# Optimization experiments

Measured on AMD Instinct MI355X. Metric: run time of the kernel, lower is better.

Reference implementation:

```python
import jax, jax.numpy as jnp
import numpy as np

HIDDEN = 768
HEADS = 12
HEAD_DIM = 64
SEQ = 512
DS_K = 64  # downsampling_k
EPS = 1e-6


def setup_inputs() -> dict:
    key = jax.random.key(0)
    ks = jax.random.split(key, 16)
    B = 32
    sd = 1.0 / DS_K
    glorot = jax.nn.initializers.lecun_normal()  # flax default_kernel_init
    inp = {
        "query": jax.random.normal(ks[0], (B, SEQ, HIDDEN), jnp.float32),
        "key": jax.random.normal(ks[1], (B, SEQ, HIDDEN), jnp.float32),
        "value": jax.random.normal(ks[2], (B, SEQ, HIDDEN), jnp.float32),
        "step": 0,
        # learned Linformer-style downsampling projections [k, s]
        "W_kds": sd * jax.random.normal(ks[3], (DS_K, SEQ), jnp.float32),
        "W_vds": sd * jax.random.normal(ks[4], (DS_K, SEQ), jnp.float32),
        # DenseGeneral qkv kernels [d, n, h] and biases [n, h]
        "Wq": glorot(ks[5], (HIDDEN, HEADS, HEAD_DIM), jnp.float32),
        "bq": jnp.zeros((HEADS, HEAD_DIM), jnp.float32),
        "Wk": glorot(ks[6], (HIDDEN, HEADS, HEAD_DIM), jnp.float32),
        "bk": jnp.zeros((HEADS, HEAD_DIM), jnp.float32),
        "Wv": glorot(ks[7], (HIDDEN, HEADS, HEAD_DIM), jnp.float32),
        "bv": jnp.zeros((HEADS, HEAD_DIM), jnp.float32),
        # out projection contracts (n, h) -> hidden
        "Wout": glorot(ks[8], (HEADS * HEAD_DIM, HIDDEN), jnp.float32).reshape(HEADS, HEAD_DIM, HIDDEN),
        "bout": jnp.zeros((HIDDEN,), jnp.float32),
    }
    return inp


def reference(query, key, value, step, W_kds, W_vds, Wq, bq, Wk, bk, Wv, bv, Wout, bout):
    # Linformer-style downsample of keys/values along sequence: [b,s,d] -> [b,k,d]
    key_ds = jnp.einsum("ks,bsd->bkd", W_kds, key)
    val_ds = jnp.einsum("ks,bsd->bkd", W_vds, value)

    # per-head projections
    queries = jnp.einsum("bqd,dnh->bqnh", query, Wq) + bq    # [b,q,n,h]
    keys = jnp.einsum("bkd,dnh->bknh", key_ds, Wk) + bk      # [b,k,n,h]
    values = jnp.einsum("bkd,dnh->bknh", val_ds, Wv) + bv    # [b,k,n,h]

    # kernelized linear attention with elu feature map (mask=False path)
    phi_q = jax.nn.elu(queries) + 1.0
    phi_k = jax.nn.elu(keys) + 1.0
    s = jnp.einsum("bknd,bknh->bndh", phi_k, values)          # [b,n,h,h] KV state
    z = jnp.sum(phi_k, axis=1)                                 # [b,n,h]
    qs = jnp.einsum("bqnd,bndh->bqnh", phi_q, s)
    qz = jnp.einsum("bqnd,bnd->bqn", phi_q, z) + EPS
    a_v = qs / qz[..., None]                                   # [b,q,n,h]

    out = jnp.einsum("bqnh,nhD->bqD", a_v, Wout) + bout        # [b,q,hidden]
    return out
```

## Files before the change

### kernel.cpp

```cpp
#include <hip/hip_runtime.h>

typedef unsigned short u16;
typedef u16 u16x4 __attribute__((ext_vector_type(4)));
typedef u16 u16x8 __attribute__((ext_vector_type(8)));
typedef __bf16 bf16;
typedef bf16 bf16x8 __attribute__((ext_vector_type(8)));
typedef float f32x4 __attribute__((ext_vector_type(4)));

__device__ __forceinline__ float bf2f(u16 v) {
  union { unsigned u; float f; } x; x.u = ((unsigned)v) << 16; return x.f;
}
__device__ __forceinline__ u16 f2bf(float f) {
  union { float f; unsigned u; } x; x.f = f;
  unsigned u = x.u;
  u += 0x7fffu + ((u >> 16) & 1u);
  return (u16)(u >> 16);
}
__device__ __forceinline__ unsigned cvt2bf(float lo, float hi) {
  unsigned r;
  asm("v_cvt_pk_bf16_f32 %0, %1, %2" : "=v"(r) : "v"(lo), "v"(hi));
  return r;
}

#define GLDS16(g, l) __builtin_amdgcn_global_load_lds( \
    (const __attribute__((address_space(1))) unsigned int*)(const void*)(g), \
    (__attribute__((address_space(3))) unsigned int*)(void*)(l), 16, 0, 0)

__global__ __launch_bounds__(256) void prep_k(
    const float* __restrict__ Wq, const float* __restrict__ Wk,
    const float* __restrict__ Wv, const float* __restrict__ Wout,
    const float* __restrict__ wkds, const float* __restrict__ wvds,
    const float* __restrict__ b0, const float* __restrict__ b1,
    const float* __restrict__ b2, const float* __restrict__ b3,
    u16* __restrict__ WT, u16* __restrict__ dstW, u16* __restrict__ dstB)
{
  __shared__ u16 T[64][72];
  const int blk = blockIdx.x;
  const int t = threadIdx.x;
  if (blk < 576) {
    const int bz = blk / 144, rr = blk % 144;
    const int r0 = (rr / 12) * 64, c0 = (rr % 12) * 64;
    const float* W = (bz == 0) ? Wq : (bz == 1) ? Wk : (bz == 2) ? Wv : Wout;
    u16* O = WT + (size_t)bz * 768 * 768;
    #pragma unroll
    for (int p = 0; p < 2; ++p) {
      int v = t + p * 256;
      int r = v / 8, c = (v % 8) * 8;
      f32x4 x0 = *(const f32x4*)&W[(size_t)(r0 + r) * 768 + c0 + c];
      f32x4 x1 = *(const f32x4*)&W[(size_t)(r0 + r) * 768 + c0 + c + 4];
      #pragma unroll
      for (int i = 0; i < 4; ++i) { T[r][c + i] = f2bf(x0[i]); T[r][c + 4 + i] = f2bf(x1[i]); }
    }
    __syncthreads();
    #pragma unroll
    for (int p = 0; p < 2; ++p) {
      int v = t + p * 256;
      int r = v / 8, c = (v % 8) * 8;
      u16x8 tv;
      #pragma unroll
      for (int i = 0; i < 8; ++i) tv[i] = T[c + i][r];
      *(u16x8*)&O[(size_t)(c0 + r) * 768 + r0 + c] = tv;
    }
  } else if (blk < 832) {
    const int i = (blk - 576) * 256 + t;
    if (i < 32768) dstW[i] = f2bf(wkds[i]);
    else           dstW[i] = f2bf(wvds[i - 32768]);
  } else {
    const int i = (blk - 832) * 256 + t;
    if (i < 3072) {
      int s = i / 768, si = i % 768;
      const float* src = (s == 0) ? b0 : (s == 1) ? b1 : (s == 2) ? b2 : b3;
      dstB[i] = f2bf(src[si]);
    }
  }
}

__global__ __launch_bounds__(256) void ds_k(
    const u16* __restrict__ Wds,
    const float* __restrict__ key, const float* __restrict__ value,
    u16* __restrict__ key_ds)
{
  __shared__ u16 Bs[2][64 * 40];
  const int pair = blockIdx.y >> 5, b = blockIdx.y & 31;
  const float* src = (pair ? value : key) + (size_t)b * 512 * 768;
  const u16* W = Wds + pair * 32768;
  u16* dst = key_ds + (size_t)pair * 1572864 + (size_t)b * 49152;
  const int nt = blockIdx.x * 64;
  const int t = threadIdx.x, wave = t >> 6, lane = t & 63;
  const int wm = (wave >> 1) * 32, wn = (wave & 1) * 32;
  const int lrow = lane & 15, quad = lane >> 4;
  const int bn = t & 63, bk8 = (t >> 6) * 8;
  const float* bcol = src + nt + bn;

  f32x4 acc[2][2] = {};
  float breg[8];
  bf16x8 av[2][2];

  #pragma unroll
  for (int i = 0; i < 8; ++i) breg[i] = bcol[(size_t)(bk8 + i) * 768];
  #pragma unroll
  for (int i = 0; i < 2; ++i)
    av[0][i] = *(const bf16x8*)&W[(size_t)(wm + i * 16 + lrow) * 512 + quad * 8];

  #pragma unroll
  for (int step = 0; step < 16; ++step) {
    const int cur = step & 1, nxt = cur ^ 1;
    u16x8 wv;
    #pragma unroll
    for (int i = 0; i < 8; ++i) wv[i] = f2bf(breg[i]);
    *(u16x8*)&Bs[cur][bn * 40 + bk8] = wv;
    if (step < 15) {
      const int k1 = (step + 1) * 32;
      #pragma unroll
      for (int i = 0; i < 8; ++i) breg[i] = bcol[(size_t)(k1 + bk8 + i) * 768];
      #pragma unroll
      for (int i = 0; i < 2; ++i)
        av[nxt][i] = *(const bf16x8*)&W[(size_t)(wm + i * 16 + lrow) * 512 + k1 + quad * 8];
    }
    __syncthreads();
    bf16x8 bv[2];
    #pragma unroll
    for (int j = 0; j < 2; ++j)
      bv[j] = *(const bf16x8*)&Bs[cur][(wn + j * 16 + lrow) * 40 + quad * 8];
    #pragma unroll
    for (int i = 0; i < 2; ++i)
      #pragma unroll
      for (int j = 0; j < 2; ++j)
        acc[i][j] = __builtin_amdgcn_mfma_f32_16x16x32_bf16(av[cur][i], bv[j], acc[i][j], 0, 0, 0);
  }

  #pragma unroll
  for (int i = 0; i < 2; ++i)
    #pragma unroll
    for (int j = 0; j < 2; ++j) {
      const int col = nt + wn + j * 16 + lrow;
      #pragma unroll
      for (int r = 0; r < 4; ++r) {
        const int row = wm + i * 16 + quad * 4 + r;
        dst[(size_t)row * 768 + col] = f2bf(acc[i][j][r]);
      }
    }
}

__global__ __launch_bounds__(256) void gemmqf_k(
    const float* __restrict__ A, const u16* __restrict__ Bt,
    u16* __restrict__ C, const u16* __restrict__ bias)
{
  __shared__ float As[128 * 32];
  __shared__ u16 Bs[128 * 32];
  const int blk = blockIdx.x;
  const int wg = (blk & 7) * 96 + (blk >> 3);
  const int mt = (wg / 6) * 128, nt = (wg % 6) * 128;
  const int t = threadIdx.x, wave = t >> 6, lane = t & 63;
  const int wm = (wave >> 1) * 64, wn = (wave & 1) * 64;
  const int lrow = lane & 15, quad = lane >> 4;
  f32x4 acc[4][4] = {};

  for (int k0 = 0; k0 < 768; k0 += 32) {
    __syncthreads();
    #pragma unroll
    for (int p = 0; p < 4; ++p) {
      const int idx = wave * 256 + p * 64 + lane;
      const int r = idx >> 3, ch = idx & 7;
      const int chs = ch ^ (r & 7);
      GLDS16(&A[(size_t)(mt + r) * 768 + k0 + chs * 4], &As[(wave * 256 + p * 64) * 4]);
    }
    #pragma unroll
    for (int p = 0; p < 2; ++p) {
      const int s = wave * 128 + p * 64 + lane;
      const int r = s >> 2, c = (s & 3) * 8;
      GLDS16(&Bt[(size_t)(nt + r) * 768 + k0 + c], &Bs[(wave * 128 + p * 64) * 8]);
    }
    __syncthreads();

    bf16x8 av[4], bv[4];
    #pragma unroll
    for (int i = 0; i < 4; ++i) {
      const int row = wm + i * 16 + lrow;
      f32x4 a0 = *(const f32x4*)&As[row * 32 + ((2 * quad) ^ (row & 7)) * 4];
      f32x4 a1 = *(const f32x4*)&As[row * 32 + ((2 * quad + 1) ^ (row & 7)) * 4];
      union { unsigned w[4]; bf16x8 v; } cv;
      cv.w[0] = cvt2bf(a0[0], a0[1]); cv.w[1] = cvt2bf(a0[2], a0[3]);
      cv.w[2] = cvt2bf(a1[0], a1[1]); cv.w[3] = cvt2bf(a1[2], a1[3]);
      av[i] = cv.v;
    }
    #pragma unroll
    for (int j = 0; j < 4; ++j) bv[j] = *(const bf16x8*)&Bs[(wn + j * 16 + lrow) * 32 + quad * 8];
    #pragma unroll
    for (int i = 0; i < 4; ++i)
      #pragma unroll
      for (int j = 0; j < 4; ++j)
        acc[i][j] = __builtin_amdgcn_mfma_f32_16x16x32_bf16(av[i], bv[j], acc[i][j], 0, 0, 0);
  }

  #pragma unroll
  for (int i = 0; i < 4; ++i) {
    #pragma unroll
    for (int j = 0; j < 4; ++j) {
      const int col = nt + wn + j * 16 + lrow;
      const float badd = bf2f(bias[col]);
      #pragma unroll
      for (int r = 0; r < 4; ++r) {
        const int row = mt + wm + i * 16 + quad * 4 + r;
        float v = acc[i][j][r] + badd;
        v = v > 0.0f ? v + 1.0f : __expf(v);
        C[(size_t)row * 768 + col] = f2bf(v);
      }
    }
  }
}

template<int ACT, bool OF32>
__global__ __launch_bounds__(256) void gemm97_k(
    const u16* __restrict__ A, int lda,
    const u16* __restrict__ Bt, int ldb,
    void* __restrict__ Craw, int ldc,
    const u16* __restrict__ bias, int K)
{
  __shared__ u16 As[128 * 32];
  __shared__ u16 Bs[128 * 32];
  const int blk = blockIdx.x;
  const int wg = (blk & 7) * 96 + (blk >> 3);
  const int mt = (wg / 6) * 128, nt = (wg % 6) * 128;
  const int t = threadIdx.x, wave = t >> 6, lane = t & 63;
  const int wm = (wave >> 1) * 64, wn = (wave & 1) * 64;
  const int lrow = lane & 15, quad = lane >> 4;
  f32x4 acc[4][4] = {};

  for (int k0 = 0; k0 < K; k0 += 32) {
    __syncthreads();
    #pragma unroll
    for (int p = 0; p < 2; ++p) {
      const int s = wave * 128 + p * 64 + lane;
      const int r = s >> 2, c = (s & 3) * 8;
      const int lb = (wave * 128 + p * 64) * 8;
      GLDS16(&A[(size_t)(mt + r) * lda + k0 + c], &As[lb]);
      GLDS16(&Bt[(size_t)(nt + r) * ldb + k0 + c], &Bs[lb]);
    }
    __syncthreads();

    bf16x8 av[4], bv[4];
    #pragma unroll
    for (int i = 0; i < 4; ++i) av[i] = *(const bf16x8*)&As[(wm + i * 16 + lrow) * 32 + quad * 8];
    #pragma unroll
    for (int j = 0; j < 4; ++j) bv[j] = *(const bf16x8*)&Bs[(wn + j * 16 + lrow) * 32 + quad * 8];
    #pragma unroll
    for (int i = 0; i < 4; ++i)
      #pragma unroll
      for (int j = 0; j < 4; ++j)
        acc[i][j] = __builtin_amdgcn_mfma_f32_16x16x32_bf16(av[i], bv[j], acc[i][j], 0, 0, 0);
  }

  #pragma unroll
  for (int i = 0; i < 4; ++i) {
    #pragma unroll
    for (int j = 0; j < 4; ++j) {
      const int col = nt + wn + j * 16 + lrow;
      const float badd = bias ? bf2f(bias[col]) : 0.0f;
      #pragma unroll
      for (int r = 0; r < 4; ++r) {
        const int row = mt + wm + i * 16 + quad * 4 + r;
        float v = acc[i][j][r] + badd;
        if constexpr (ACT == 1) v = v > 0.0f ? v + 1.0f : __expf(v);
        if constexpr (OF32) ((float*)Craw)[(size_t)row * ldc + col] = v;
        else                ((u16*)Craw)[(size_t)row * ldc + col] = f2bf(v);
      }
    }
  }
}

__global__ __launch_bounds__(256) void fkv_k(
    const u16* __restrict__ key_ds,
    const u16* __restrict__ WT,
    const u16* __restrict__ bias_c,
    u16* __restrict__ sT, float* __restrict__ z)
{
  __shared__ char sm[32768];
  u16* T0 = (u16*)sm;
  u16* Pt = (u16*)sm;
  u16* Vt = (u16*)(sm + 9216);
  const int x = blockIdx.x;
  const int b = x / 12, n = x % 12;
  const int t = threadIdx.x, wave = t >> 6, lane = t & 63;
  const u16* srcs[4] = {
    key_ds + (size_t)b * 49152,
    WT + 589824 + (size_t)n * 49152,
    key_ds + 1572864 + (size_t)b * 49152,
    WT + 2 * 589824 + (size_t)n * 49152 };
  const int grow = lane >> 3;
  const int gchunk = (lane & 7) ^ (grow & 7);
  const int isV = wave & 1;
  const int wm = (wave >> 1) * 32;
  u16* Atile = T0 + (isV ? 2 : 0) * 4096;
  u16* Btile = T0 + (isV ? 3 : 1) * 4096;
  const int lrow = lane & 15, quad = lane >> 4;
  f32x4 acc[2][4] = {};

  for (int k0 = 0; k0 < 768; k0 += 64) {
    const u16* s = srcs[wave];
    u16* dtile = T0 + wave * 4096;
    #pragma unroll
    for (int j = 0; j < 8; ++j) {
      const u16* gsrc = s + (size_t)(j * 8 + grow) * 768 + k0 + gchunk * 8;
      GLDS16(gsrc, (char*)dtile + j * 1024);
    }
    __syncthreads();
    #pragma unroll
    for (int c = 0; c < 2; ++c) {
      bf16x8 av[2], bv[4];
      #pragma unroll
      for (int i = 0; i < 2; ++i) {
        const int row = wm + i * 16 + lrow;
        av[i] = *(const bf16x8*)&Atile[row * 64 + (((c * 4 + quad) ^ (row & 7)) * 8)];
      }
      #pragma unroll
      for (int j = 0; j < 4; ++j) {
        const int row = j * 16 + lrow;
        bv[j] = *(const bf16x8*)&Btile[row * 64 + (((c * 4 + quad) ^ (row & 7)) * 8)];
      }
      #pragma unroll
      for (int i = 0; i < 2; ++i)
        #pragma unroll
        for (int j = 0; j < 4; ++j)
          acc[i][j] = __builtin_amdgcn_mfma_f32_16x16x32_bf16(av[i], bv[j], acc[i][j], 0, 0, 0);
    }
    __syncthreads();
  }

  const u16* bias = bias_c + (isV ? 1536 : 768) + n * 64;
  u16* Ttile = isV ? Vt : Pt;
  #pragma unroll
  for (int i = 0; i < 2; ++i)
    #pragma unroll
    for (int j = 0; j < 4; ++j) {
      const int col = j * 16 + lrow;
      const float badd = bf2f(bias[col]);
      u16x4 pk4;
      #pragma unroll
      for (int r = 0; r < 4; ++r) {
        float v = acc[i][j][r] + badd;
        if (!isV) v = v > 0.0f ? v + 1.0f : __expf(v);
        pk4[r] = f2bf(v);
      }
      *(u16x4*)&Ttile[col * 72 + wm + i * 16 + quad * 4] = pk4;
    }
  __syncthreads();

  const int wm2 = (wave >> 1) * 32, wn2 = (wave & 1) * 32;
  f32x4 a2[2][2] = {};
  #pragma unroll
  for (int c = 0; c < 2; ++c) {
    bf16x8 av[2], bv[2];
    #pragma unroll
    for (int i = 0; i < 2; ++i)
      av[i] = *(const bf16x8*)&Vt[(wm2 + i * 16 + lrow) * 72 + c * 32 + quad * 8];
    #pragma unroll
    for (int j = 0; j < 2; ++j)
      bv[j] = *(const bf16x8*)&Pt[(wn2 + j * 16 + lrow) * 72 + c * 32 + quad * 8];
    #pragma unroll
    for (int i = 0; i < 2; ++i)
      #pragma unroll
      for (int j = 0; j < 2; ++j)
        a2[i][j] = __builtin_amdgcn_mfma_f32_16x16x32_bf16(av[i], bv[j], a2[i][j], 0, 0, 0);
  }
  u16* sTg = sT + (size_t)x * 4096;
  #pragma unroll
  for (int i = 0; i < 2; ++i)
    #pragma unroll
    for (int j = 0; j < 2; ++j)
      #pragma unroll
      for (int r = 0; r < 4; ++r)
        sTg[(size_t)(wm2 + i * 16 + quad * 4 + r) * 64 + wn2 + j * 16 + lrow] = f2bf(a2[i][j][r]);
  if (t < 64) {
    float zz = 0.f;
    #pragma unroll
    for (int g = 0; g < 8; ++g) {
      u16x8 p = *(const u16x8*)&Pt[t * 72 + g * 8];
      #pragma unroll
      for (int e = 0; e < 8; ++e) zz += bf2f(p[e]);
    }
    z[(size_t)x * 64 + t] = zz;
  }
}

__global__ __launch_bounds__(256) void attn_av_k(
    u16* __restrict__ phi_q, const u16* __restrict__ sT, const float* __restrict__ zbuf)
{
  __shared__ u16 As[64 * 72];
  __shared__ u16 Bs[64 * 72];
  __shared__ float zv[64];
  __shared__ float zpart[4][64];
  __shared__ float zq[64];
  const int x = blockIdx.x, y = blockIdx.y;
  const int b = y / 12, n = y % 12;
  const int t = threadIdx.x;
  u16* Abase = phi_q + (size_t)b * 512 * 768 + (size_t)x * 64 * 768 + n * 64;
  const u16* Bbase = sT + (size_t)y * 4096;
  if (t < 64) zv[t] = zbuf[(size_t)y * 64 + t];
  #pragma unroll
  for (int p = 0; p < 2; ++p) {
    int v = t + p * 256;
    int r = v >> 3, c = (v & 7) * 8;
    *(u16x8*)&As[r * 72 + c] = *(const u16x8*)&Abase[(size_t)r * 768 + c];
    *(u16x8*)&Bs[r * 72 + c] = *(const u16x8*)&Bbase[r * 64 + c];
  }
  __syncthreads();
  {
    int r = t & 63, seg = t >> 6;
    float s = 0.f;
    #pragma unroll
    for (int j = 0; j < 16; ++j) s += bf2f(As[r * 72 + seg * 16 + j]) * zv[seg * 16 + j];
    zpart[seg][r] = s;
  }
  __syncthreads();
  if (t < 64) {
    float s = zpart[0][t] + zpart[1][t] + zpart[2][t] + zpart[3][t];
    zq[t] = 1.0f / (s + 1e-6f);
  }
  const int wave = t >> 6, lane = t & 63;
  const int wm = (wave >> 1) * 32, wn = (wave & 1) * 32;
  const int lrow = lane & 15, quad = lane >> 4;
  f32x4 acc[2][2] = {};
  #pragma unroll
  for (int c = 0; c < 2; ++c) {
    bf16x8 av[2], bv[2];
    #pragma unroll
    for (int i = 0; i < 2; ++i) av[i] = *(const bf16x8*)&As[(wm + i * 16 + lrow) * 72 + c * 32 + quad * 8];
    #pragma unroll
    for (int j = 0; j < 2; ++j) bv[j] = *(const bf16x8*)&Bs[(wn + j * 16 + lrow) * 72 + c * 32 + quad * 8];
    #pragma unroll
    for (int i = 0; i < 2; ++i)
      #pragma unroll
      for (int j = 0; j < 2; ++j)
        acc[i][j] = __builtin_amdgcn_mfma_f32_16x16x32_bf16(av[i], bv[j], acc[i][j], 0, 0, 0);
  }
  __syncthreads();
  #pragma unroll
  for (int i = 0; i < 2; ++i)
    #pragma unroll
    for (int j = 0; j < 2; ++j) {
      const int col = wn + j * 16 + lrow;
      #pragma unroll
      for (int r = 0; r < 4; ++r) {
        const int row = wm + i * 16 + quad * 4 + r;
        Abase[(size_t)row * 768 + col] = f2bf(acc[i][j][r] * zq[row]);
      }
    }
}

__global__ void tagfill_k(float* out, float val, int n) {
  int i = blockIdx.x * 256 + threadIdx.x;
  if (i < n) out[i] = val;
}

extern "C" void kernel_launch(void* const* d_in, const int* in_sizes, int n_in,
                              void* d_out, int out_size, void* d_ws, size_t ws_size,
                              hipStream_t stream) {
  (void)out_size;
  float* out = (float*)d_out;

  int o;
  if (n_in >= 14 && in_sizes[3] == 1) o = 4;
  else if (n_in == 13) o = 3;
  else { tagfill_k<<<4, 256, 0, stream>>>(out, 77.0f, 1024); return; }
  if (in_sizes[0] != 12582912 || in_sizes[o + 0] != 32768 || in_sizes[o + 2] != 589824) {
    tagfill_k<<<4, 256, 0, stream>>>(out, 88.0f, 1024); return;
  }

  const float* query = (const float*)d_in[0];
  const float* key   = (const float*)d_in[1];
  const float* value = (const float*)d_in[2];
  const float* W_kds = (const float*)d_in[o + 0];
  const float* W_vds = (const float*)d_in[o + 1];
  const float* Wq   = (const float*)d_in[o + 2];
  const float* bq   = (const float*)d_in[o + 3];
  const float* Wk   = (const float*)d_in[o + 4];
  const float* bk   = (const float*)d_in[o + 5];
  const float* Wv   = (const float*)d_in[o + 6];
  const float* bv   = (const float*)d_in[o + 7];
  const float* Wout = (const float*)d_in[o + 8];
  const float* bout = (const float*)d_in[o + 9];

  const size_t NEED = 61478912;
  if (ws_size < NEED) { tagfill_k<<<4, 256, 0, stream>>>(out, 123.0f, 1024); return; }

  char* base = (char*)d_ws;
  u16*   WT     = (u16*)base;
  char*  Breg   = base + 4718592;
  u16*   sT     = (u16*)Breg;
  float* zbuf   = (float*)(Breg + 3145728);
  u16*   phi_q  = (u16*)(base + 29884416);
  u16*   bias_c = (u16*)(base + 55181312);
  u16*   key_ds = (u16*)(base + 55187456);
  u16*   Wds_c  = (u16*)(base + 55050240);
  u16* a_v = phi_q;
  u16* WqT   = WT;
  u16* WoutT = WT + 3 * 768 * 768;
  u16* bq_c = bias_c, *bout_c = bias_c + 2304;

  prep_k<<<844, 256, 0, stream>>>(Wq, Wk, Wv, Wout, W_kds, W_vds,
                                  bq, bk, bv, bout, WT, Wds_c, bias_c);

  gemmqf_k<<<768, 256, 0, stream>>>(query, WqT, phi_q, bq_c);

  ds_k<<<dim3(12, 64), 256, 0, stream>>>(Wds_c, key, value, key_ds);

  fkv_k<<<384, 256, 0, stream>>>(key_ds, WT, bias_c, sT, zbuf);

  attn_av_k<<<dim3(8, 384), 256, 0, stream>>>(phi_q, sT, zbuf);

  gemm97_k<0, true><<<768, 256, 0, stream>>>(
      a_v, 768, WoutT, 768, out, 768, bout_c, 768);
}
```

Baseline: 307.7 us.

## Unify Q and output GEMMs into double-buffered register-staged kernel with BK=64

Replaces the two single-buffered GEMM kernels (direct global-to-LDS loads, two barriers per 32-wide k step) with one templated kernel. It prefetches the next 64-wide k tile into registers while MFMAs run on the current LDS buffer, then stores into a swizzled second buffer. This halves the barrier count and overlaps global latency with compute. It also adds a barrier that waits only on lgkmcnt instead of the full __syncthreads. The cost is double the LDS use (64KB per block) and more registers, which may lower occupancy.

```diff
diff --git a/kernel.cpp b/kernel.cpp
--- a/kernel.cpp
+++ b/kernel.cpp
@@ -20,6 +20,11 @@
   unsigned r;
   asm("v_cvt_pk_bf16_f32 %0, %1, %2" : "=v"(r) : "v"(lo), "v"(hi));
   return r;
+}
+
+__device__ __forceinline__ void bar_lgkm() {
+  asm volatile("s_waitcnt lgkmcnt(0)" ::: "memory");
+  __builtin_amdgcn_s_barrier();
 }
 
 #define GLDS16(g, l) __builtin_amdgcn_global_load_lds( \
@@ -117,7 +122,7 @@
       for (int i = 0; i < 2; ++i)
         av[nxt][i] = *(const bf16x8*)&W[(size_t)(wm + i * 16 + lrow) * 512 + k1 + quad * 8];
     }
-    __syncthreads();
+    bar_lgkm();
     bf16x8 bv[2];
     #pragma unroll
     for (int j = 0; j < 2; ++j)
@@ -142,55 +147,95 @@
     }
 }
 
-__global__ __launch_bounds__(256) void gemmqf_k(
-    const float* __restrict__ A, const u16* __restrict__ Bt,
-    u16* __restrict__ C, const u16* __restrict__ bias)
+template<bool AF32, int ACT, bool OF32>
+__global__ __launch_bounds__(256) void gemmdb_k(
+    const void* __restrict__ Araw, const u16* __restrict__ Bt,
+    void* __restrict__ Craw, const u16* __restrict__ bias)
 {
-  __shared__ float As[128 * 32];
-  __shared__ u16 Bs[128 * 32];
+  __shared__ u16 As[2][128 * 64];
+  __shared__ u16 Bs[2][128 * 64];
   const int blk = blockIdx.x;
   const int wg = (blk & 7) * 96 + (blk >> 3);
   const int mt = (wg / 6) * 128, nt = (wg % 6) * 128;
   const int t = threadIdx.x, wave = t >> 6, lane = t & 63;
   const int wm = (wave >> 1) * 64, wn = (wave & 1) * 64;
   const int lrow = lane & 15, quad = lane >> 4;
+  const int sr = t >> 1, sh = (t & 1) * 4;
+  const float* A32 = (const float*)Araw;
+  const u16*   A16 = (const u16*)Araw;
   f32x4 acc[4][4] = {};
 
-  for (int k0 = 0; k0 < 768; k0 += 32) {
-    __syncthreads();
-    #pragma unroll
-    for (int p = 0; p < 4; ++p) {
-      const int idx = wave * 256 + p * 64 + lane;
-      const int r = idx >> 3, ch = idx & 7;
-      const int chs = ch ^ (r & 7);
-      GLDS16(&A[(size_t)(mt + r) * 768 + k0 + chs * 4], &As[(wave * 256 + p * 64) * 4]);
-    }
-    #pragma unroll
-    for (int p = 0; p < 2; ++p) {
-      const int s = wave * 128 + p * 64 + lane;
-      const int r = s >> 2, c = (s & 3) * 8;
-      GLDS16(&Bt[(size_t)(nt + r) * 768 + k0 + c], &Bs[(wave * 128 + p * 64) * 8]);
-    }
-    __syncthreads();
-
-    bf16x8 av[4], bv[4];
-    #pragma unroll
-    for (int i = 0; i < 4; ++i) {
-      const int row = wm + i * 16 + lrow;
-      f32x4 a0 = *(const f32x4*)&As[row * 32 + ((2 * quad) ^ (row & 7)) * 4];
-      f32x4 a1 = *(const f32x4*)&As[row * 32 + ((2 * quad + 1) ^ (row & 7)) * 4];
-      union { unsigned w[4]; bf16x8 v; } cv;
-      cv.w[0] = cvt2bf(a0[0], a0[1]); cv.w[1] = cvt2bf(a0[2], a0[3]);
-      cv.w[2] = cvt2bf(a1[0], a1[1]); cv.w[3] = cvt2bf(a1[2], a1[3]);
-      av[i] = cv.v;
-    }
-    #pragma unroll
-    for (int j = 0; j < 4; ++j) bv[j] = *(const bf16x8*)&Bs[(wn + j * 16 + lrow) * 32 + quad * 8];
-    #pragma unroll
-    for (int i = 0; i < 4; ++i)
-      #pragma unroll
-      for (int j = 0; j < 4; ++j)
-        acc[i][j] = __builtin_amdgcn_mfma_f32_16x16x32_bf16(av[i], bv[j], acc[i][j], 0, 0, 0);
+  f32x4 ar[8];
+  u16x8 ar16[4];
+  u16x8 br[4];
+
+  auto loadAB = [&](int k0) {
+    if constexpr (AF32) {
+      #pragma unroll
+      for (int g = 0; g < 4; ++g) {
+        ar[g * 2]     = *(const f32x4*)&A32[(size_t)(mt + sr) * 768 + k0 + (sh + g) * 8];
+        ar[g * 2 + 1] = *(const f32x4*)&A32[(size_t)(mt + sr) * 768 + k0 + (sh + g) * 8 + 4];
+      }
+    } else {
+      #pragma unroll
+      for (int g = 0; g < 4; ++g)
+        ar16[g] = *(const u16x8*)&A16[(size_t)(mt + sr) * 768 + k0 + (sh + g) * 8];
+    }
+    #pragma unroll
+    for (int g = 0; g < 4; ++g)
+      br[g] = *(const u16x8*)&Bt[(size_t)(nt + sr) * 768 + k0 + (sh + g) * 8];
+  };
+  auto storeAB = [&](int buf) {
+    #pragma unroll
+    for (int g = 0; g < 4; ++g) {
+      u16x8 w;
+      if constexpr (AF32) {
+        union { unsigned u[4]; u16x8 v; } cv;
+        cv.u[0] = cvt2bf(ar[g * 2][0], ar[g * 2][1]);
+        cv.u[1] = cvt2bf(ar[g * 2][2], ar[g * 2][3]);
+        cv.u[2] = cvt2bf(ar[g * 2 + 1][0], ar[g * 2 + 1][1]);
+        cv.u[3] = cvt2bf(ar[g * 2 + 1][2], ar[g * 2 + 1][3]);
+        w = cv.v;
+      } else {
+        w = ar16[g];
+      }
+      const int pos = sr * 64 + (((sh + g) ^ (sr & 7)) * 8);
+      *(u16x8*)&As[buf][pos] = w;
+      *(u16x8*)&Bs[buf][pos] = br[g];
+    }
+  };
+
+  loadAB(0);
+  storeAB(0);
+  bar_lgkm();
+
+  int cur = 0;
+  for (int ks = 0; ks < 12; ++ks) {
+    if (ks < 11) loadAB((ks + 1) * 64);
+    #pragma unroll
+    for (int c = 0; c < 2; ++c) {
+      bf16x8 av[4], bv[4];
+      #pragma unroll
+      for (int i = 0; i < 4; ++i) {
+        const int row = wm + i * 16 + lrow;
+        av[i] = *(const bf16x8*)&As[cur][row * 64 + (((c * 4 + quad) ^ (row & 7)) * 8)];
+      }
+      #pragma unroll
+      for (int j = 0; j < 4; ++j) {
+        const int row = wn + j * 16 + lrow;
+        bv[j] = *(const bf16x8*)&Bs[cur][row * 64 + (((c * 4 + quad) ^ (row & 7)) * 8)];
+      }
+      #pragma unroll
+      for (int i = 0; i < 4; ++i)
+        #pragma unroll
+        for (int j = 0; j < 4; ++j)
+          acc[i][j] = __builtin_amdgcn_mfma_f32_16x16x32_bf16(av[i], bv[j], acc[i][j], 0, 0, 0);
+    }
+    if (ks < 11) {
+      storeAB(cur ^ 1);
+      bar_lgkm();
+      cur ^= 1;
+    }
   }
 
   #pragma unroll
@@ -199,71 +244,13 @@
     for (int j = 0; j < 4; ++j) {
       const int col = nt + wn + j * 16 + lrow;
       const float badd = bf2f(bias[col]);
-      #pragma unroll
-      for (int r = 0; r < 4; ++r) {
-        const int row = mt + wm + i * 16 + quad * 4 + r;
-        float v = acc[i][j][r] + badd;
-        v = v > 0.0f ? v + 1.0f : __expf(v);
-        C[(size_t)row * 768 + col] = f2bf(v);
-      }
-    }
-  }
-}
-
-template<int ACT, bool OF32>
-__global__ __launch_bounds__(256) void gemm97_k(
-    const u16* __restrict__ A, int lda,
-    const u16* __restrict__ Bt, int ldb,
-    void* __restrict__ Craw, int ldc,
-    const u16* __restrict__ bias, int K)
-{
-  __shared__ u16 As[128 * 32];
-  __shared__ u16 Bs[128 * 32];
-  const int blk = blockIdx.x;
-  const int wg = (blk & 7) * 96 + (blk >> 3);
-  const int mt = (wg / 6) * 128, nt = (wg % 6) * 128;
-  const int t = threadIdx.x, wave = t >> 6, lane = t & 63;
-  const int wm = (wave >> 1) * 64, wn = (wave & 1) * 64;
-  const int lrow = lane & 15, quad = lane >> 4;
-  f32x4 acc[4][4] = {};
-
-  for (int k0 = 0; k0 < K; k0 += 32) {
-    __syncthreads();
-    #pragma unroll
-    for (int p = 0; p < 2; ++p) {
-      const int s = wave * 128 + p * 64 + lane;
-      const int r = s >> 2, c = (s & 3) * 8;
-      const int lb = (wave * 128 + p * 64) * 8;
-      GLDS16(&A[(size_t)(mt + r) * lda + k0 + c], &As[lb]);
-      GLDS16(&Bt[(size_t)(nt + r) * ldb + k0 + c], &Bs[lb]);
-    }
-    __syncthreads();
-
-    bf16x8 av[4], bv[4];
-    #pragma unroll
-    for (int i = 0; i < 4; ++i) av[i] = *(const bf16x8*)&As[(wm + i * 16 + lrow) * 32 + quad * 8];
-    #pragma unroll
-    for (int j = 0; j < 4; ++j) bv[j] = *(const bf16x8*)&Bs[(wn + j * 16 + lrow) * 32 + quad * 8];
-    #pragma unroll
-    for (int i = 0; i < 4; ++i)
-      #pragma unroll
-      for (int j = 0; j < 4; ++j)
-        acc[i][j] = __builtin_amdgcn_mfma_f32_16x16x32_bf16(av[i], bv[j], acc[i][j], 0, 0, 0);
-  }
-
-  #pragma unroll
-  for (int i = 0; i < 4; ++i) {
-    #pragma unroll
-    for (int j = 0; j < 4; ++j) {
-      const int col = nt + wn + j * 16 + lrow;
-      const float badd = bias ? bf2f(bias[col]) : 0.0f;
       #pragma unroll
       for (int r = 0; r < 4; ++r) {
         const int row = mt + wm + i * 16 + quad * 4 + r;
         float v = acc[i][j][r] + badd;
         if constexpr (ACT == 1) v = v > 0.0f ? v + 1.0f : __expf(v);
-        if constexpr (OF32) ((float*)Craw)[(size_t)row * ldc + col] = v;
-        else                ((u16*)Craw)[(size_t)row * ldc + col] = f2bf(v);
+        if constexpr (OF32) ((float*)Craw)[(size_t)row * 768 + col] = v;
+        else                ((u16*)Craw)[(size_t)row * 768 + col] = f2bf(v);
       }
     }
   }
@@ -501,7 +488,7 @@
   prep_k<<<844, 256, 0, stream>>>(Wq, Wk, Wv, Wout, W_kds, W_vds,
                                   bq, bk, bv, bout, WT, Wds_c, bias_c);
 
-  gemmqf_k<<<768, 256, 0, stream>>>(query, WqT, phi_q, bq_c);
+  gemmdb_k<true, 1, false><<<768, 256, 0, stream>>>(query, WqT, phi_q, bq_c);
 
   ds_k<<<dim3(12, 64), 256, 0, stream>>>(Wds_c, key, value, key_ds);
 
@@ -509,6 +496,5 @@
 
   attn_av_k<<<dim3(8, 384), 256, 0, stream>>>(phi_q, sT, zbuf);
 
-  gemm97_k<0, true><<<768, 256, 0, stream>>>(
-      a_v, 768, WoutT, 768, out, 768, bout_c, 768);
-}
+  gemmdb_k<false, 0, true><<<768, 256, 0, stream>>>(a_v, WoutT, out, bout_c);
+}
```

After: 329.4 us. 1.07x slower.
